# Performance work log

Measured on AMD Instinct MI355X. Metric: run time of the kernel, lower is better.

## Reference

```python
import jax, jax.numpy as jnp
import numpy as np

HEAD_SIZE = 64
INPUT_SIZE = 1024
B, T = 4, 4096


def setup_inputs() -> dict:
    key = jax.random.key(0)
    ks = jax.random.split(key, 7)
    s = 1.0 / np.sqrt(INPUT_SIZE)
    return {
        "x": jax.random.normal(ks[0], (B, T, INPUT_SIZE), dtype=jnp.float32),
        "Wk": jax.random.uniform(ks[1], (INPUT_SIZE, HEAD_SIZE), jnp.float32, -s, s),
        "bk": jax.random.uniform(ks[2], (HEAD_SIZE,), jnp.float32, -s, s),
        "Wq": jax.random.uniform(ks[3], (INPUT_SIZE, HEAD_SIZE), jnp.float32, -s, s),
        "bq": jax.random.uniform(ks[4], (HEAD_SIZE,), jnp.float32, -s, s),
        "Wv": jax.random.uniform(ks[5], (INPUT_SIZE, HEAD_SIZE), jnp.float32, -s, s),
        "bv": jax.random.uniform(ks[6], (HEAD_SIZE,), jnp.float32, -s, s),
    }


def reference(x, Wk, bk, Wq, bq, Wv, bv) -> jnp.ndarray:
    # x: [B, T, D]
    Tlen = x.shape[1]
    k = x @ Wk + bk          # [B, T, H]
    q = x @ Wq + bq          # [B, T, H]
    v = x @ Wv + bv          # [B, T, H]
    scale = 1.0 / jnp.sqrt(jnp.float32(HEAD_SIZE))
    # NOTE: original computes k @ q^T (not q @ k^T) -- keep that exact math.
    w = jnp.einsum("bth,bsh->bts", k, q) * scale  # [B, T, T]
    causal = jnp.tril(jnp.ones((Tlen, Tlen), dtype=bool))
    w = jnp.where(causal, w, -jnp.inf)
    w = jax.nn.softmax(w, axis=-1)
    out = jnp.einsum("bts,bsh->bth", w, v)        # [B, T, H]
    return out
```

## Files before the change

### kernel.cpp

```cpp
#include <hip/hip_runtime.h>
#include <hip/hip_bf16.h>
#include <stdint.h>

typedef __attribute__((ext_vector_type(8))) short short8;
typedef __attribute__((ext_vector_type(4))) float floatx4;

#define HD 64
#define D_IN 1024
#define TLEN 4096
#define NB 4
#define PPB 288
#define LDP 72

__device__ __forceinline__ short f2bf(float f) {
    union { float f; uint32_t u; } v{f};
    uint32_t u = v.u;
    uint32_t r = (u + 0x7FFFu + ((u >> 16) & 1u)) >> 16;
    return (short)r;
}

__device__ __forceinline__ uint32_t pk2(float a, float b) {
    __hip_bfloat162 h = __float22bfloat162_rn(float2{a, b});
    union { __hip_bfloat162 h; uint32_t u; } c{h};
    return c.u;
}

__device__ __forceinline__ void ld_lds16(const void* g, void* l) {
    __builtin_amdgcn_global_load_lds(
        (const __attribute__((address_space(1))) uint32_t*)g,
        (__attribute__((address_space(3))) uint32_t*)l, 16, 0, 0);
}

__global__ __launch_bounds__(256) void prep_w(const float* __restrict__ Wk,
                                              const float* __restrict__ Wq,
                                              const float* __restrict__ Wv,
                                              short* __restrict__ wt) {
    int i = blockIdx.x * 256 + threadIdx.x;
    int j  = i & 7;
    int l  = (i >> 3) & 63;
    int ks = (i >> 9) & 1;
    int rest = i >> 10;
    int f  = rest % 12;
    int kt = rest / 12;
    int mat = f >> 2, nt = f & 3;
    int n = nt * 16 + (l & 15);
    int k = kt * 64 + ks * 32 + (l >> 4) * 8 + j;
    const float* W = (mat == 0) ? Wk : ((mat == 1) ? Wq : Wv);
    wt[i] = f2bf(W[(size_t)k * 64 + n]);
}

__global__ __launch_bounds__(256) void proj(const float* __restrict__ x,
                                            const float* __restrict__ bk,
                                            const float* __restrict__ bq,
                                            const float* __restrict__ bv,
                                            const short* __restrict__ wt,
                                            short* __restrict__ ko,
                                            short* __restrict__ qo,
                                            short* __restrict__ vt) {
    __shared__ float xs[2][4096];
    __shared__ short ws2[2][12288];

    int tid = threadIdx.x;
    int wave = tid >> 6, lane = tid & 63;
    int quad = lane >> 4, l16 = lane & 15;
    int row0 = blockIdx.x * 64;
    int wbase = tid & ~63;

    floatx4 acc[4][3];
#pragma unroll
    for (int mt = 0; mt < 4; mt++)
#pragma unroll
        for (int fi = 0; fi < 3; fi++) acc[mt][fi] = (floatx4){0.f, 0.f, 0.f, 0.f};

    auto stage = [&](int kt, int buf) {
#pragma unroll
        for (int it = 0; it < 4; it++) {
            int s = it * 256 + tid;
            int r = s >> 4, p = s & 15;
            int c = (((p >> 1) ^ (r & 7)) << 1) | (p & 1);
            ld_lds16(x + (size_t)(row0 + r) * D_IN + kt * 64 + c * 4,
                     &xs[buf][(it * 256 + wbase) * 4]);
        }
#pragma unroll
        for (int it = 0; it < 6; it++) {
            int s = it * 256 + tid;
            ld_lds16(wt + (size_t)kt * 12288 + (size_t)s * 8,
                     &ws2[buf][(it * 256 + wbase) * 8]);
        }
    };

    stage(0, 0);
    for (int kt = 0; kt < 16; kt++) {
        int buf = kt & 1;
        __syncthreads();
        if (kt < 15) stage(kt + 1, buf ^ 1);
#pragma unroll
        for (int ks = 0; ks < 2; ks++) {
            short8 av[4];
#pragma unroll
            for (int mt = 0; mt < 4; mt++) {
                int r = mt * 16 + l16;
                int g = ks * 4 + quad;
                const float4* pp = reinterpret_cast<const float4*>(
                    &xs[buf][r * 64 + ((g ^ (r & 7)) << 1) * 4]);
                float4 f0 = pp[0], f1 = pp[1];
                union { uint32_t u[4]; short8 s; } cv;
                cv.u[0] = pk2(f0.x, f0.y); cv.u[1] = pk2(f0.z, f0.w);
                cv.u[2] = pk2(f1.x, f1.y); cv.u[3] = pk2(f1.z, f1.w);
                av[mt] = cv.s;
            }
#pragma unroll
            for (int fi = 0; fi < 3; fi++) {
                int f = wave * 3 + fi;
                short8 bf = *reinterpret_cast<const short8*>(
                    &ws2[buf][((f * 2 + ks) * 64 + lane) * 8]);
#pragma unroll
                for (int mt = 0; mt < 4; mt++)
                    acc[mt][fi] = __builtin_amdgcn_mfma_f32_16x16x32_bf16(av[mt], bf, acc[mt][fi], 0, 0, 0);
            }
        }
    }

#pragma unroll
    for (int fi = 0; fi < 3; fi++) {
        int f = wave * 3 + fi;
        int mat = f >> 2, nt = f & 3;
        int col = nt * 16 + l16;
        const float* bias = (mat == 0) ? bk : ((mat == 1) ? bq : bv);
        float bb = bias[col];
#pragma unroll
        for (int mt = 0; mt < 4; mt++)
#pragma unroll
            for (int reg = 0; reg < 4; reg++) {
                float v = acc[mt][fi][reg] + bb;
                int row = row0 + mt * 16 + quad * 4 + reg;
                if (mat == 0) ko[(size_t)row * HD + col] = f2bf(v);
                else if (mat == 1) qo[(size_t)row * HD + col] = f2bf(v);
                else {
                    int bt = row >> 12, tl = row & 4095;
                    vt[(size_t)bt * HD * TLEN + (size_t)col * TLEN + tl] = f2bf(v);
                }
            }
    }
}

template<int SPLIT>
__global__ __launch_bounds__(256) void attn_kern(const short* __restrict__ kb,
                                                 const short* __restrict__ qb,
                                                 const short* __restrict__ vtw,
                                                 float* __restrict__ dst,
                                                 float* __restrict__ pL) {
    __shared__ short Ks[2][4096];
    __shared__ short Vs[2][4096];
    __shared__ short Ps[64 * LDP];

    int tid = threadIdx.x;
    int wave = tid >> 6, lane = tid & 63;
    int quad = lane >> 4, l16 = lane & 15;
    int wbase = tid & ~63;
    int batch = blockIdx.y;

    int tile, j0, j1, slot = 0;
    if (SPLIT) {
        int bx = blockIdx.x;
        int t = 0, accb = 0;
        for (;;) { int p = (t + 8) >> 3; if (bx < accb + p) break; accb += p; ++t; }
        tile = t;
        j0 = (bx - accb) * 8;
        int je = j0 + 8, lim = tile + 1;
        j1 = je < lim ? je : lim;
        slot = batch * PPB + bx;
    } else {
        tile = 63 - blockIdx.x;
        j0 = 0; j1 = tile + 1;
    }
    int t0 = tile * 64;
    size_t base = (size_t)batch * TLEN * HD;
    const short* vbase = vtw + (size_t)batch * HD * TLEN;

    short8 qf[2];
    {
        int trow = t0 + wave * 16 + l16;
#pragma unroll
        for (int ks = 0; ks < 2; ks++)
            qf[ks] = *reinterpret_cast<const short8*>(kb + base + (size_t)trow * HD + ks * 32 + quad * 8);
    }

    floatx4 o_acc[4];
#pragma unroll
    for (int ht = 0; ht < 4; ht++) o_acc[ht] = (floatx4){0.f, 0.f, 0.f, 0.f};
    float l_sum[4] = {0.f, 0.f, 0.f, 0.f};
    const float sl2e = 0.18033688011112042f;

    auto stage = [&](int j, int buf) {
        int s0 = j * 64;
#pragma unroll
        for (int it = 0; it < 2; it++) {
            int s = it * 256 + tid;
            int r = s >> 3, c = (s & 7) ^ (r & 7);
            ld_lds16(qb + base + (size_t)(s0 + r) * HD + c * 8,
                     &Ks[buf][(it * 256 + wbase) * 8]);
            ld_lds16(vbase + (size_t)r * TLEN + s0 + c * 8,
                     &Vs[buf][(it * 256 + wbase) * 8]);
        }
    };

    stage(j0, 0);
    for (int j = j0; j < j1; ++j) {
        int buf = (j - j0) & 1;
        __syncthreads();
        if (j + 1 < j1) stage(j + 1, buf ^ 1);

        int s0 = j * 64;
        floatx4 sacc[4];
#pragma unroll
        for (int nt = 0; nt < 4; nt++) sacc[nt] = (floatx4){0.f, 0.f, 0.f, 0.f};
#pragma unroll
        for (int ks = 0; ks < 2; ks++)
#pragma unroll
            for (int nt = 0; nt < 4; nt++) {
                int r = nt * 16 + l16, g = ks * 4 + quad;
                short8 b = *reinterpret_cast<const short8*>(
                    &Ks[buf][r * 64 + (g ^ (r & 7)) * 8]);
                sacc[nt] = __builtin_amdgcn_mfma_f32_16x16x32_bf16(qf[ks], b, sacc[nt], 0, 0, 0);
            }

        bool diag = (j == tile);
        float pv[4][4];
#pragma unroll
        for (int nt = 0; nt < 4; nt++) {
            int s_g = s0 + nt * 16 + l16;
#pragma unroll
            for (int reg = 0; reg < 4; reg++) {
                float p = __builtin_amdgcn_exp2f(sacc[nt][reg] * sl2e);
                if (diag && s_g > t0 + wave * 16 + quad * 4 + reg) p = 0.f;
                pv[nt][reg] = p;
            }
        }
#pragma unroll
        for (int reg = 0; reg < 4; reg++) {
            float s = (pv[0][reg] + pv[1][reg]) + (pv[2][reg] + pv[3][reg]);
#pragma unroll
            for (int off = 8; off >= 1; off >>= 1) s += __shfl_xor(s, off, 16);
            l_sum[reg] += s;
        }
#pragma unroll
        for (int nt = 0; nt < 4; nt++)
#pragma unroll
            for (int reg = 0; reg < 4; reg++)
                Ps[(wave * 16 + quad * 4 + reg) * LDP + nt * 16 + l16] = f2bf(pv[nt][reg]);

#pragma unroll
        for (int ks = 0; ks < 2; ks++) {
            short8 a = *reinterpret_cast<const short8*>(&Ps[(wave * 16 + l16) * LDP + ks * 32 + quad * 8]);
#pragma unroll
            for (int ht = 0; ht < 4; ht++) {
                int r = ht * 16 + l16, g = ks * 4 + quad;
                short8 b = *reinterpret_cast<const short8*>(
                    &Vs[buf][r * 64 + (g ^ (r & 7)) * 8]);
                o_acc[ht] = __builtin_amdgcn_mfma_f32_16x16x32_bf16(a, b, o_acc[ht], 0, 0, 0);
            }
        }
    }

    if (SPLIT) {
        float* po = dst + (size_t)slot * 4096;
#pragma unroll
        for (int ht = 0; ht < 4; ht++)
#pragma unroll
            for (int reg = 0; reg < 4; reg++)
                po[(wave * 16 + quad * 4 + reg) * 64 + ht * 16 + l16] = o_acc[ht][reg];
#pragma unroll
        for (int reg = 0; reg < 4; reg++)
            if (l16 == reg) pL[(size_t)slot * 64 + wave * 16 + quad * 4 + reg] = l_sum[reg];
    } else {
        float inv[4];
#pragma unroll
        for (int reg = 0; reg < 4; reg++) inv[reg] = 1.0f / l_sum[reg];
#pragma unroll
        for (int ht = 0; ht < 4; ht++)
#pragma unroll
            for (int reg = 0; reg < 4; reg++)
                dst[base + (size_t)(t0 + wave * 16 + quad * 4 + reg) * HD + ht * 16 + l16] =
                    o_acc[ht][reg] * inv[reg];
    }
}

__global__ __launch_bounds__(256) void attn_combine(const float* __restrict__ pO,
                                                    const float* __restrict__ pL,
                                                    float* __restrict__ out) {
    int tile = blockIdx.x, batch = blockIdx.y;
    int nparts = (tile + 8) >> 3;
    int g = tile >> 3, r = tile & 7;
    int slot0 = batch * PPB + 4 * g * (g + 1) + r * (g + 1);
    int t = threadIdx.x;
    int row = t >> 2;

    float L = 0.f;
    float4 acc[4];
#pragma unroll
    for (int i = 0; i < 4; i++) acc[i] = (float4){0.f, 0.f, 0.f, 0.f};

    for (int p = 0; p < nparts; ++p) {
        int slot = slot0 + p;
        L += pL[(size_t)slot * 64 + row];
        const float4* src = reinterpret_cast<const float4*>(pO + (size_t)slot * 4096 + (size_t)t * 16);
#pragma unroll
        for (int i = 0; i < 4; i++) {
            float4 v = src[i];
            acc[i].x += v.x; acc[i].y += v.y; acc[i].z += v.z; acc[i].w += v.w;
        }
    }
    float inv = 1.0f / L;
    float4* dstp = reinterpret_cast<float4*>(out + (size_t)batch * TLEN * HD +
                                             (size_t)tile * 64 * HD + (size_t)t * 16);
#pragma unroll
    for (int i = 0; i < 4; i++) {
        float4 v; v.x = acc[i].x * inv; v.y = acc[i].y * inv; v.z = acc[i].z * inv; v.w = acc[i].w * inv;
        dstp[i] = v;
    }
}

extern "C" void kernel_launch(void* const* d_in, const int* in_sizes, int n_in,
                              void* d_out, int out_size, void* d_ws, size_t ws_size,
                              hipStream_t stream) {
    const float* x  = (const float*)d_in[0];
    const float* Wk = (const float*)d_in[1];
    const float* bk = (const float*)d_in[2];
    const float* Wq = (const float*)d_in[3];
    const float* bq = (const float*)d_in[4];
    const float* Wv = (const float*)d_in[5];
    const float* bv = (const float*)d_in[6];
    float* out = (float*)d_out;

    const size_t nrow = (size_t)NB * TLEN;
    short* ko = (short*)d_ws;
    short* qo = ko + nrow * HD;
    short* vt = qo + nrow * HD;
    short* wt = vt + nrow * HD;
    float* pO = (float*)(wt + 3 * 64 * 1024);
    float* pL = pO + (size_t)NB * PPB * 4096;
    size_t need = (size_t)((char*)(pL + (size_t)NB * PPB * 64) - (char*)d_ws);

    prep_w<<<768, 256, 0, stream>>>(Wk, Wq, Wv, wt);
    proj<<<256, 256, 0, stream>>>(x, bk, bq, bv, wt, ko, qo, vt);
    if (ws_size >= need) {
        attn_kern<1><<<dim3(PPB, NB), 256, 0, stream>>>(ko, qo, vt, pO, pL);
        attn_combine<<<dim3(64, NB), 256, 0, stream>>>(pO, pL, out);
    } else {
        attn_kern<0><<<dim3(64, NB), 256, 0, stream>>>(ko, qo, vt, out, nullptr);
    }
}
```

Baseline: 164.4 us.

## Use 128-row query tiles in attention, halve projection tile, fold softmax scale into K

Each attention block now handles 128 query rows, with two 16-row MFMA subtiles per wave, so every staged K/V tile is reused twice and the number of split partitions per batch drops. The softmax scale times log2(e) is folded into the K projection output, which removes a multiply per score. The row-sum shuffle reduction moves out of the inner loop to the epilogue. The projection kernel uses 32-row tiles over twice as many blocks to spread work across more CUs, at the cost of more register use in attention and fewer, larger blocks there.

```diff
diff --git a/kernel.cpp b/kernel.cpp
--- a/kernel.cpp
+++ b/kernel.cpp
@@ -9,8 +9,9 @@
 #define D_IN 1024
 #define TLEN 4096
 #define NB 4
-#define PPB 288
+#define PPB 144
 #define LDP 72
+#define SL2E 0.18033688011112042f
 
 __device__ __forceinline__ short f2bf(float f) {
     union { float f; uint32_t u; } v{f};
@@ -57,24 +58,24 @@
                                             short* __restrict__ ko,
                                             short* __restrict__ qo,
                                             short* __restrict__ vt) {
-    __shared__ float xs[2][4096];
+    __shared__ float xs[2][2048];
     __shared__ short ws2[2][12288];
 
     int tid = threadIdx.x;
     int wave = tid >> 6, lane = tid & 63;
     int quad = lane >> 4, l16 = lane & 15;
-    int row0 = blockIdx.x * 64;
+    int row0 = blockIdx.x * 32;
     int wbase = tid & ~63;
 
-    floatx4 acc[4][3];
-#pragma unroll
-    for (int mt = 0; mt < 4; mt++)
+    floatx4 acc[2][3];
+#pragma unroll
+    for (int mt = 0; mt < 2; mt++)
 #pragma unroll
         for (int fi = 0; fi < 3; fi++) acc[mt][fi] = (floatx4){0.f, 0.f, 0.f, 0.f};
 
     auto stage = [&](int kt, int buf) {
 #pragma unroll
-        for (int it = 0; it < 4; it++) {
+        for (int it = 0; it < 2; it++) {
             int s = it * 256 + tid;
             int r = s >> 4, p = s & 15;
             int c = (((p >> 1) ^ (r & 7)) << 1) | (p & 1);
@@ -96,9 +97,9 @@
         if (kt < 15) stage(kt + 1, buf ^ 1);
 #pragma unroll
         for (int ks = 0; ks < 2; ks++) {
-            short8 av[4];
-#pragma unroll
-            for (int mt = 0; mt < 4; mt++) {
+            short8 av[2];
+#pragma unroll
+            for (int mt = 0; mt < 2; mt++) {
                 int r = mt * 16 + l16;
                 int g = ks * 4 + quad;
                 const float4* pp = reinterpret_cast<const float4*>(
@@ -115,7 +116,7 @@
                 short8 bf = *reinterpret_cast<const short8*>(
                     &ws2[buf][((f * 2 + ks) * 64 + lane) * 8]);
 #pragma unroll
-                for (int mt = 0; mt < 4; mt++)
+                for (int mt = 0; mt < 2; mt++)
                     acc[mt][fi] = __builtin_amdgcn_mfma_f32_16x16x32_bf16(av[mt], bf, acc[mt][fi], 0, 0, 0);
             }
         }
@@ -129,12 +130,12 @@
         const float* bias = (mat == 0) ? bk : ((mat == 1) ? bq : bv);
         float bb = bias[col];
 #pragma unroll
-        for (int mt = 0; mt < 4; mt++)
+        for (int mt = 0; mt < 2; mt++)
 #pragma unroll
             for (int reg = 0; reg < 4; reg++) {
                 float v = acc[mt][fi][reg] + bb;
                 int row = row0 + mt * 16 + quad * 4 + reg;
-                if (mat == 0) ko[(size_t)row * HD + col] = f2bf(v);
+                if (mat == 0) ko[(size_t)row * HD + col] = f2bf(v * SL2E);
                 else if (mat == 1) qo[(size_t)row * HD + col] = f2bf(v);
                 else {
                     int bt = row >> 12, tl = row & 4095;
@@ -152,7 +153,7 @@
                                                  float* __restrict__ pL) {
     __shared__ short Ks[2][4096];
     __shared__ short Vs[2][4096];
-    __shared__ short Ps[64 * LDP];
+    __shared__ short Ps[128 * LDP];
 
     int tid = threadIdx.x;
     int wave = tid >> 6, lane = tid & 63;
@@ -164,33 +165,36 @@
     if (SPLIT) {
         int bx = blockIdx.x;
         int t = 0, accb = 0;
-        for (;;) { int p = (t + 8) >> 3; if (bx < accb + p) break; accb += p; ++t; }
+        for (;;) { int p = (2 * t + 9) >> 3; if (bx < accb + p) break; accb += p; ++t; }
         tile = t;
         j0 = (bx - accb) * 8;
-        int je = j0 + 8, lim = tile + 1;
+        int je = j0 + 8, lim = 2 * tile + 2;
         j1 = je < lim ? je : lim;
         slot = batch * PPB + bx;
     } else {
-        tile = 63 - blockIdx.x;
-        j0 = 0; j1 = tile + 1;
-    }
-    int t0 = tile * 64;
+        tile = 31 - blockIdx.x;
+        j0 = 0; j1 = 2 * tile + 2;
+    }
+    int t0 = tile * 128;
+    int jd = 2 * tile;
     size_t base = (size_t)batch * TLEN * HD;
     const short* vbase = vtw + (size_t)batch * HD * TLEN;
 
-    short8 qf[2];
-    {
-        int trow = t0 + wave * 16 + l16;
+    short8 qf[2][2];
+#pragma unroll
+    for (int mt = 0; mt < 2; mt++) {
+        int trow = t0 + wave * 32 + mt * 16 + l16;
 #pragma unroll
         for (int ks = 0; ks < 2; ks++)
-            qf[ks] = *reinterpret_cast<const short8*>(kb + base + (size_t)trow * HD + ks * 32 + quad * 8);
-    }
-
-    floatx4 o_acc[4];
-#pragma unroll
-    for (int ht = 0; ht < 4; ht++) o_acc[ht] = (floatx4){0.f, 0.f, 0.f, 0.f};
-    float l_sum[4] = {0.f, 0.f, 0.f, 0.f};
-    const float sl2e = 0.18033688011112042f;
+            qf[mt][ks] = *reinterpret_cast<const short8*>(kb + base + (size_t)trow * HD + ks * 32 + quad * 8);
+    }
+
+    floatx4 o_acc[2][4];
+#pragma unroll
+    for (int mt = 0; mt < 2; mt++)
+#pragma unroll
+        for (int ht = 0; ht < 4; ht++) o_acc[mt][ht] = (floatx4){0.f, 0.f, 0.f, 0.f};
+    float l_p[2][4] = {{0.f,0.f,0.f,0.f},{0.f,0.f,0.f,0.f}};
 
     auto stage = [&](int j, int buf) {
         int s0 = j * 64;
@@ -211,10 +215,11 @@
         __syncthreads();
         if (j + 1 < j1) stage(j + 1, buf ^ 1);
 
-        int s0 = j * 64;
-        floatx4 sacc[4];
-#pragma unroll
-        for (int nt = 0; nt < 4; nt++) sacc[nt] = (floatx4){0.f, 0.f, 0.f, 0.f};
+        floatx4 sacc[2][4];
+#pragma unroll
+        for (int mt = 0; mt < 2; mt++)
+#pragma unroll
+            for (int nt = 0; nt < 4; nt++) sacc[mt][nt] = (floatx4){0.f, 0.f, 0.f, 0.f};
 #pragma unroll
         for (int ks = 0; ks < 2; ks++)
 #pragma unroll
@@ -222,67 +227,103 @@
                 int r = nt * 16 + l16, g = ks * 4 + quad;
                 short8 b = *reinterpret_cast<const short8*>(
                     &Ks[buf][r * 64 + (g ^ (r & 7)) * 8]);
-                sacc[nt] = __builtin_amdgcn_mfma_f32_16x16x32_bf16(qf[ks], b, sacc[nt], 0, 0, 0);
-            }
-
-        bool diag = (j == tile);
-        float pv[4][4];
-#pragma unroll
-        for (int nt = 0; nt < 4; nt++) {
-            int s_g = s0 + nt * 16 + l16;
-#pragma unroll
-            for (int reg = 0; reg < 4; reg++) {
-                float p = __builtin_amdgcn_exp2f(sacc[nt][reg] * sl2e);
-                if (diag && s_g > t0 + wave * 16 + quad * 4 + reg) p = 0.f;
-                pv[nt][reg] = p;
-            }
-        }
-#pragma unroll
-        for (int reg = 0; reg < 4; reg++) {
-            float s = (pv[0][reg] + pv[1][reg]) + (pv[2][reg] + pv[3][reg]);
-#pragma unroll
-            for (int off = 8; off >= 1; off >>= 1) s += __shfl_xor(s, off, 16);
-            l_sum[reg] += s;
-        }
-#pragma unroll
-        for (int nt = 0; nt < 4; nt++)
+#pragma unroll
+                for (int mt = 0; mt < 2; mt++)
+                    sacc[mt][nt] = __builtin_amdgcn_mfma_f32_16x16x32_bf16(qf[mt][ks], b, sacc[mt][nt], 0, 0, 0);
+            }
+
+        float pv[2][4][4];
+#pragma unroll
+        for (int mt = 0; mt < 2; mt++)
+#pragma unroll
+            for (int nt = 0; nt < 4; nt++)
+#pragma unroll
+                for (int reg = 0; reg < 4; reg++)
+                    pv[mt][nt][reg] = __builtin_amdgcn_exp2f(sacc[mt][nt][reg]);
+        if (j >= jd) {
+            int s0 = j * 64;
+#pragma unroll
+            for (int mt = 0; mt < 2; mt++) {
+                int tg = t0 + wave * 32 + mt * 16 + quad * 4;
+#pragma unroll
+                for (int nt = 0; nt < 4; nt++) {
+                    int s_g = s0 + nt * 16 + l16;
+#pragma unroll
+                    for (int reg = 0; reg < 4; reg++)
+                        if (s_g > tg + reg) pv[mt][nt][reg] = 0.f;
+                }
+            }
+        }
+#pragma unroll
+        for (int mt = 0; mt < 2; mt++)
 #pragma unroll
             for (int reg = 0; reg < 4; reg++)
-                Ps[(wave * 16 + quad * 4 + reg) * LDP + nt * 16 + l16] = f2bf(pv[nt][reg]);
+                l_p[mt][reg] += (pv[mt][0][reg] + pv[mt][1][reg]) + (pv[mt][2][reg] + pv[mt][3][reg]);
+#pragma unroll
+        for (int mt = 0; mt < 2; mt++)
+#pragma unroll
+            for (int nt = 0; nt < 4; nt++)
+#pragma unroll
+                for (int reg = 0; reg < 4; reg++)
+                    Ps[(wave * 32 + mt * 16 + quad * 4 + reg) * LDP + nt * 16 + l16] = f2bf(pv[mt][nt][reg]);
 
 #pragma unroll
         for (int ks = 0; ks < 2; ks++) {
-            short8 a = *reinterpret_cast<const short8*>(&Ps[(wave * 16 + l16) * LDP + ks * 32 + quad * 8]);
+            short8 a[2];
+#pragma unroll
+            for (int mt = 0; mt < 2; mt++)
+                a[mt] = *reinterpret_cast<const short8*>(
+                    &Ps[(wave * 32 + mt * 16 + l16) * LDP + ks * 32 + quad * 8]);
 #pragma unroll
             for (int ht = 0; ht < 4; ht++) {
                 int r = ht * 16 + l16, g = ks * 4 + quad;
                 short8 b = *reinterpret_cast<const short8*>(
                     &Vs[buf][r * 64 + (g ^ (r & 7)) * 8]);
-                o_acc[ht] = __builtin_amdgcn_mfma_f32_16x16x32_bf16(a, b, o_acc[ht], 0, 0, 0);
-            }
-        }
-    }
+#pragma unroll
+                for (int mt = 0; mt < 2; mt++)
+                    o_acc[mt][ht] = __builtin_amdgcn_mfma_f32_16x16x32_bf16(a[mt], b, o_acc[mt][ht], 0, 0, 0);
+            }
+        }
+    }
+
+#pragma unroll
+    for (int mt = 0; mt < 2; mt++)
+#pragma unroll
+        for (int reg = 0; reg < 4; reg++) {
+            float s = l_p[mt][reg];
+#pragma unroll
+            for (int off = 8; off >= 1; off >>= 1) s += __shfl_xor(s, off, 16);
+            l_p[mt][reg] = s;
+        }
 
     if (SPLIT) {
-        float* po = dst + (size_t)slot * 4096;
-#pragma unroll
-        for (int ht = 0; ht < 4; ht++)
+        float* po = dst + (size_t)slot * 8192;
+#pragma unroll
+        for (int mt = 0; mt < 2; mt++)
+#pragma unroll
+            for (int ht = 0; ht < 4; ht++)
+#pragma unroll
+                for (int reg = 0; reg < 4; reg++) {
+                    int lr = wave * 32 + mt * 16 + quad * 4 + reg;
+                    po[lr * 64 + ht * 16 + l16] = o_acc[mt][ht][reg];
+                }
+#pragma unroll
+        for (int mt = 0; mt < 2; mt++)
 #pragma unroll
             for (int reg = 0; reg < 4; reg++)
-                po[(wave * 16 + quad * 4 + reg) * 64 + ht * 16 + l16] = o_acc[ht][reg];
-#pragma unroll
-        for (int reg = 0; reg < 4; reg++)
-            if (l16 == reg) pL[(size_t)slot * 64 + wave * 16 + quad * 4 + reg] = l_sum[reg];
+                if (l16 == mt * 4 + reg)
+                    pL[(size_t)slot * 128 + wave * 32 + mt * 16 + quad * 4 + reg] = l_p[mt][reg];
     } else {
-        float inv[4];
-#pragma unroll
-        for (int reg = 0; reg < 4; reg++) inv[reg] = 1.0f / l_sum[reg];
-#pragma unroll
-        for (int ht = 0; ht < 4; ht++)
-#pragma unroll
-            for (int reg = 0; reg < 4; reg++)
-                dst[base + (size_t)(t0 + wave * 16 + quad * 4 + reg) * HD + ht * 16 + l16] =
-                    o_acc[ht][reg] * inv[reg];
+#pragma unroll
+        for (int mt = 0; mt < 2; mt++)
+#pragma unroll
+            for (int reg = 0; reg < 4; reg++) {
+                float inv = 1.0f / l_p[mt][reg];
+                int t = t0 + wave * 32 + mt * 16 + quad * 4 + reg;
+#pragma unroll
+                for (int ht = 0; ht < 4; ht++)
+                    dst[base + (size_t)t * HD + ht * 16 + l16] = o_acc[mt][ht][reg] * inv;
+            }
     }
 }
 
@@ -290,32 +331,33 @@
                                                     const float* __restrict__ pL,
                                                     float* __restrict__ out) {
     int tile = blockIdx.x, batch = blockIdx.y;
-    int nparts = (tile + 8) >> 3;
-    int g = tile >> 3, r = tile & 7;
-    int slot0 = batch * PPB + 4 * g * (g + 1) + r * (g + 1);
+    int nparts = (2 * tile + 9) >> 3;
+    int a = tile >> 2, r = tile & 3;
+    int slot0 = batch * PPB + 2 * a * (a + 1) + r * (a + 1);
     int t = threadIdx.x;
-    int row = t >> 2;
+    int off = t * 32;
+    int row = off >> 6;
 
     float L = 0.f;
-    float4 acc[4];
-#pragma unroll
-    for (int i = 0; i < 4; i++) acc[i] = (float4){0.f, 0.f, 0.f, 0.f};
+    float4 acc[8];
+#pragma unroll
+    for (int i = 0; i < 8; i++) acc[i] = (float4){0.f, 0.f, 0.f, 0.f};
 
     for (int p = 0; p < nparts; ++p) {
         int slot = slot0 + p;
-        L += pL[(size_t)slot * 64 + row];
-        const float4* src = reinterpret_cast<const float4*>(pO + (size_t)slot * 4096 + (size_t)t * 16);
-#pragma unroll
-        for (int i = 0; i < 4; i++) {
+        L += pL[(size_t)slot * 128 + row];
+        const float4* src = reinterpret_cast<const float4*>(pO + (size_t)slot * 8192 + off);
+#pragma unroll
+        for (int i = 0; i < 8; i++) {
             float4 v = src[i];
             acc[i].x += v.x; acc[i].y += v.y; acc[i].z += v.z; acc[i].w += v.w;
         }
     }
     float inv = 1.0f / L;
     float4* dstp = reinterpret_cast<float4*>(out + (size_t)batch * TLEN * HD +
-                                             (size_t)tile * 64 * HD + (size_t)t * 16);
-#pragma unroll
-    for (int i = 0; i < 4; i++) {
+                                             (size_t)tile * 128 * HD + off);
+#pragma unroll
+    for (int i = 0; i < 8; i++) {
         float4 v; v.x = acc[i].x * inv; v.y = acc[i].y * inv; v.z = acc[i].z * inv; v.w = acc[i].w * inv;
         dstp[i] = v;
     }
@@ -339,15 +381,15 @@
     short* vt = qo + nrow * HD;
     short* wt = vt + nrow * HD;
     float* pO = (float*)(wt + 3 * 64 * 1024);
-    float* pL = pO + (size_t)NB * PPB * 4096;
-    size_t need = (size_t)((char*)(pL + (size_t)NB * PPB * 64) - (char*)d_ws);
+    float* pL = pO + (size_t)NB * PPB * 8192;
+    size_t need = (size_t)((char*)(pL + (size_t)NB * PPB * 128) - (char*)d_ws);
 
     prep_w<<<768, 256, 0, stream>>>(Wk, Wq, Wv, wt);
-    proj<<<256, 256, 0, stream>>>(x, bk, bq, bv, wt, ko, qo, vt);
+    proj<<<512, 256, 0, stream>>>(x, bk, bq, bv, wt, ko, qo, vt);
     if (ws_size >= need) {
         attn_kern<1><<<dim3(PPB, NB), 256, 0, stream>>>(ko, qo, vt, pO, pL);
-        attn_combine<<<dim3(64, NB), 256, 0, stream>>>(pO, pL, out);
+        attn_combine<<<dim3(32, NB), 256, 0, stream>>>(pO, pL, out);
     } else {
-        attn_kern<0><<<dim3(64, NB), 256, 0, stream>>>(ko, qo, vt, out, nullptr);
-    }
-}
+        attn_kern<0><<<dim3(32, NB), 256, 0, stream>>>(ko, qo, vt, out, nullptr);
+    }
+}
```

Result: faster. 160.6 us (-2.3%).
